# Kernel optimization log

Measured on AMD Instinct MI355X. Metric: run time of the kernel, lower is better.

Reference implementation:

```python
import jax, jax.numpy as jnp
import numpy as np

NMUL = 1
NEARZERO = 1e-5
ROUTING_LEN = 15
N_DYN = 3
N_STATIC = 13  # layout includes parRT, parAC (present in STATIC_PARAM_NAMES but unused in the step)


def _descale(x, lb, ub):
    return lb + x * (ub - lb)


def setup_inputs() -> dict:
    key = jax.random.key(0)
    k1, k2, k3 = jax.random.split(key, 3)
    T, G = 365, 50000
    u = jax.random.uniform(k1, (T, G, 3), dtype=jnp.float32)
    prcp = u[..., 0] * 10.0                 # mm/day
    tmean = (u[..., 1] - 0.3) * 20.0        # degC, roughly [-6, 14] so snow branch is exercised
    pet = u[..., 2] * 5.0                   # mm/day
    forcing = jnp.stack([prcp, tmean, pet], axis=-1)
    dyn_raw = jax.random.uniform(k2, (T, G, N_DYN * NMUL), dtype=jnp.float32)
    static_raw = jax.random.uniform(k3, (G, N_STATIC * NMUL + 2), dtype=jnp.float32)
    return {"forcing": forcing, "dyn_raw": dyn_raw, "static_raw": static_raw}


def _hbv_forward(forcing, dyn_raw, static_raw):
    T, G, _ = forcing.shape
    dt = forcing.dtype
    # --- descale dynamic params (per-timestep): parBETA, parK0, parBETAET ---
    dyn = dyn_raw.reshape(T, G, N_DYN, NMUL)
    parBETA = _descale(dyn[:, :, 0], 1.0, 6.0)
    parK0 = _descale(dyn[:, :, 1], 0.05, 0.9)
    parBETAET = _descale(dyn[:, :, 2], 0.3, 5.0)
    # --- descale static params ---
    st = static_raw[:, :N_STATIC * NMUL].reshape(G, N_STATIC, NMUL)
    parFC = _descale(st[:, 0], 50.0, 1000.0)
    parK1 = _descale(st[:, 1], 0.01, 0.5)
    parK2 = _descale(st[:, 2], 0.001, 0.2)
    parLP = _descale(st[:, 3], 0.2, 1.0)
    parPERC = _descale(st[:, 4], 0.0, 10.0)
    parUZL = _descale(st[:, 5], 0.0, 100.0)
    parTT = _descale(st[:, 6], -2.5, 2.5)
    parCFMAX = _descale(st[:, 7], 0.5, 10.0)
    parCFR = _descale(st[:, 8], 0.0, 0.1)
    parCWH = _descale(st[:, 9], 0.0, 0.2)
    parC = _descale(st[:, 10], 0.0, 1.0)
    rout = static_raw[:, N_STATIC * NMUL:]
    rout_a = _descale(rout[:, 0], 0.0, 2.9)
    rout_b = _descale(rout[:, 1], 0.0, 6.5)

    Pm = jnp.broadcast_to(forcing[..., 0:1], (T, G, NMUL))
    Tm = jnp.broadcast_to(forcing[..., 1:2], (T, G, NMUL))
    PETm = jnp.broadcast_to(forcing[..., 2:3], (T, G, NMUL))

    def step(carry, xs):
        SNOWPACK, MELTWATER, SM, SUZ, SLZ = carry
        PRECIP, TEMP, PET, pBETA, pK0, pBETAET = xs
        is_rain = (TEMP >= parTT).astype(dt)
        RAIN = PRECIP * is_rain
        SNOW = PRECIP * (1.0 - is_rain)
        SNOWPACK = SNOWPACK + SNOW
        melt = jnp.minimum(jnp.maximum(parCFMAX * (TEMP - parTT), 0.0), SNOWPACK)
        MELTWATER = MELTWATER + melt
        SNOWPACK = SNOWPACK - melt
        refreezing = jnp.minimum(jnp.maximum(parCFR * parCFMAX * (parTT - TEMP), 0.0), MELTWATER)
        SNOWPACK = SNOWPACK + refreezing
        MELTWATER = MELTWATER - refreezing
        tosoil = jnp.maximum(MELTWATER - parCWH * SNOWPACK, 0.0)
        MELTWATER = MELTWATER - tosoil
        soil_wetness = jnp.clip((SM / parFC) ** pBETA, 0.0, 1.0)
        recharge = (RAIN + tosoil) * soil_wetness
        SM = SM + RAIN + tosoil - recharge
        excess = jnp.maximum(SM - parFC, 0.0)
        SM = SM - excess
        evapfactor = jnp.clip((SM / (parLP * parFC)) ** pBETAET, 0.0, 1.0)
        ETact = jnp.minimum(SM, PET * evapfactor)
        SM = jnp.maximum(SM - ETact, NEARZERO)
        capillary = jnp.minimum(SLZ, parC * SLZ * (1.0 - jnp.minimum(SM / parFC, 1.0)))
        SM = jnp.maximum(SM + capillary, NEARZERO)
        SLZ = jnp.maximum(SLZ - capillary, NEARZERO)
        SUZ = SUZ + recharge + excess
        PERC = jnp.minimum(SUZ, parPERC)
        SUZ = SUZ - PERC
        Q0 = pK0 * jnp.maximum(SUZ - parUZL, 0.0)
        SUZ = SUZ - Q0
        Q1 = parK1 * SUZ
        SUZ = SUZ - Q1
        SLZ = jnp.maximum(SLZ + PERC, 0.0)
        Q2 = parK2 * SLZ
        SLZ = SLZ - Q2
        return (SNOWPACK, MELTWATER, SM, SUZ, SLZ), Q0 + Q1 + Q2

    init = tuple(jnp.full((G, NMUL), 0.001, dtype=dt) for _ in range(5))
    _, Qall = jax.lax.scan(step, init, (Pm, Tm, PETm, parBETA, parK0, parBETAET))
    Qsim = Qall.mean(axis=-1)  # [T, G]: average over nmul components

    # --- gamma unit-hydrograph routing (hydroDL UH_gamma + causal conv, lenF = 15) ---
    aa = jax.nn.relu(rout_a) + 0.1      # shape param, [G]
    theta = jax.nn.relu(rout_b) + 0.5   # scale param, [G]
    t = jnp.arange(0.5, ROUTING_LEN, dtype=dt)[:, None]  # [15, 1] midpoints
    w = (t ** (aa - 1.0)) * jnp.exp(-t / theta) / (jnp.exp(jax.lax.lgamma(aa)) * theta ** aa)
    w = w / w.sum(axis=0)  # [15, G], normalized UH weights
    Qpad = jnp.pad(Qsim, ((ROUTING_LEN - 1, 0), (0, 0)))
    # causal conv: Qrout[t] = sum_k w[k] * Qsim[t-k]; fixed 15-tap loop
    Qrout = sum(w[k] * jax.lax.dynamic_slice_in_dim(Qpad, ROUTING_LEN - 1 - k, T, axis=0)
                for k in range(ROUTING_LEN))
    return Qrout  # streamflow [T, G]


def reference(forcing, dyn_raw, static_raw):
    return _hbv_forward(forcing, dyn_raw, static_raw)
```

## Files before the change

### kernel.cpp

```cpp
#include <hip/hip_runtime.h>

#define NEARZERO 1e-5f
#define RLEN 15
#define LOG2E 1.4426950408889634f

struct __attribute__((packed, aligned(4))) F3 { float x, y, z; };

static __device__ __forceinline__ F3 ld3f(const float* p) {
    return *reinterpret_cast<const F3*>(p);
}

struct Par { float FC, invFC, invLPFC, K1, K2, PERC, UZL, TT, CFMAX, CFRC, CWH, C; };

template<int PH>
__device__ __forceinline__ float one_step(
    float P, float TEMP, float PET, float dx, float dy, float dz,
    const Par& pr,
    float& SNOWPACK, float& MELTWATER, float& SM, float& SUZ, float& SLZ,
    float (&acc)[RLEN], const float (&w)[RLEN])
{
    const float pBETA   = fmaf(dx, 5.0f, 1.0f);
    const float pK0     = fmaf(dy, 0.85f, 0.05f);
    const float pBETAET = fmaf(dz, 4.7f, 0.3f);

    const float d    = TEMP - pr.TT;
    const float RAIN = (d >= 0.0f) ? P : 0.0f;
    const float SNOW = P - RAIN;
    SNOWPACK += SNOW;
    const float melt = __builtin_amdgcn_fmed3f(pr.CFMAX * d, 0.0f, SNOWPACK);
    MELTWATER += melt;
    SNOWPACK  -= melt;
    const float refr = __builtin_amdgcn_fmed3f(pr.CFRC * (0.0f - d), 0.0f, MELTWATER);
    SNOWPACK  += refr;
    MELTWATER -= refr;
    const float tosoil = fmaxf(fmaf(-pr.CWH, SNOWPACK, MELTWATER), 0.0f);
    MELTWATER -= tosoil;

    const float sw = fminf(exp2f(pBETA * __log2f(SM * pr.invFC)), 1.0f);
    const float rt = RAIN + tosoil;
    const float recharge = rt * sw;
    SM = SM + rt - recharge;
    const float excess = fmaxf(SM - pr.FC, 0.0f);
    SM -= excess;
    const float ef = fminf(exp2f(pBETAET * __log2f(SM * pr.invLPFC)), 1.0f);
    const float ETact = fminf(SM, PET * ef);
    SM = fmaxf(SM - ETact, NEARZERO);
    const float capillary = pr.C * SLZ * (1.0f - fminf(SM * pr.invFC, 1.0f));
    SM  = fmaxf(SM + capillary, NEARZERO);
    SLZ = fmaxf(SLZ - capillary, NEARZERO);

    SUZ += recharge + excess;
    const float PERC = fminf(SUZ, pr.PERC);
    SUZ -= PERC;
    const float Q0 = pK0 * fmaxf(SUZ - pr.UZL, 0.0f);
    SUZ -= Q0;
    const float Q1 = pr.K1 * SUZ;
    SUZ -= Q1;
    SLZ += PERC;
    const float Q2 = pr.K2 * SLZ;
    SLZ -= Q2;
    const float Qsim = Q0 + Q1 + Q2;

    const float qr = fmaf(w[0], Qsim, acc[PH]);
    acc[PH] = 0.0f;
#pragma unroll
    for (int k = 1; k < RLEN; ++k) {
        const int j = (PH + k) % RLEN;
        acc[j] = fmaf(w[k], Qsim, acc[j]);
    }
    return qr;
}

__global__ __launch_bounds__(64, 1) void hbv_kernel(
    const float* __restrict__ forcing,
    const float* __restrict__ dynr,
    const float* __restrict__ statr,
    float* __restrict__ out,
    int G)
{
    const int lane = threadIdx.x;
    const int g  = blockIdx.x * 64 + lane;
    const int gc = (g < G) ? g : (G - 1);
    const bool guard = (g < G);

    __shared__ float ring[RLEN][64][6];

    const float* sp = statr + (size_t)gc * 15;
    Par pr;
    pr.FC    = fmaf(sp[0], 950.0f, 50.0f);
    pr.K1    = fmaf(sp[1], 0.49f, 0.01f);
    pr.K2    = fmaf(sp[2], 0.199f, 0.001f);
    const float parLP = fmaf(sp[3], 0.8f, 0.2f);
    pr.PERC  = sp[4] * 10.0f;
    pr.UZL   = sp[5] * 100.0f;
    pr.TT    = fmaf(sp[6], 5.0f, -2.5f);
    pr.CFMAX = fmaf(sp[7], 9.5f, 0.5f);
    pr.CFRC  = (sp[8] * 0.1f) * pr.CFMAX;
    pr.CWH   = sp[9] * 0.2f;
    pr.C     = sp[10];
    const float rout_a = sp[13] * 2.9f;
    const float rout_b = sp[14] * 6.5f;
    pr.invFC   = 1.0f / pr.FC;
    pr.invLPFC = 1.0f / (parLP * pr.FC);

    const float aa    = fmaxf(rout_a, 0.0f) + 0.1f;
    const float theta = fmaxf(rout_b, 0.0f) + 0.5f;
    const float am1   = aa - 1.0f;
    const float nitl2 = -LOG2E / theta;
    float w[RLEN];
    float wsum = 0.0f;
#pragma unroll
    for (int k = 0; k < RLEN; ++k) {
        const float tk = (float)k + 0.5f;
        w[k] = exp2f(am1 * __log2f(tk) + tk * nitl2);
        wsum += w[k];
    }
    const float winv = 1.0f / wsum;
#pragma unroll
    for (int k = 0; k < RLEN; ++k) w[k] *= winv;

    float SP_ = 0.001f, MW = 0.001f, SM = 0.001f, SUZ = 0.001f, SLZ = 0.001f;
    float acc[RLEN];
#pragma unroll
    for (int k = 0; k < RLEN; ++k) acc[k] = 0.0f;

    const size_t sT = (size_t)G * 3;
    const float* pF = forcing + (size_t)gc * 3;
    const float* pD = dynr    + (size_t)gc * 3;
    float* outp = out + g;

    F3 setF[5], setD[5];

    setF[1] = ld3f(pF + 4 * sT); setD[1] = ld3f(pD + 4 * sT);
    setF[2] = ld3f(pF + 5 * sT); setD[2] = ld3f(pD + 5 * sT);
    setF[3] = ld3f(pF + 6 * sT); setD[3] = ld3f(pD + 6 * sT);
    setF[4] = ld3f(pF + 7 * sT); setD[4] = ld3f(pD + 7 * sT);
#pragma unroll
    for (int r = 0; r < 4; ++r) {
        const F3 f = ld3f(pF + (size_t)r * sT);
        const F3 d = ld3f(pD + (size_t)r * sT);
        ring[r][lane][0] = f.x; ring[r][lane][1] = f.y; ring[r][lane][2] = f.z;
        ring[r][lane][3] = d.x; ring[r][lane][4] = d.y; ring[r][lane][5] = d.z;
    }

#define STEP(PH, FP, DP) do { \
    constexpr int P_  = (PH) % RLEN; \
    constexpr int S_  = P_ % 5; \
    constexpr int Sw_ = (P_ + 1) % 5; \
    constexpr int W_  = (P_ + 4) % RLEN; \
    setF[S_] = ld3f(FP); setD[S_] = ld3f(DP); \
    __builtin_amdgcn_sched_barrier(0); \
    const float P2_ = ring[P_][lane][0], T2_ = ring[P_][lane][1], E2_ = ring[P_][lane][2]; \
    const float x2_ = ring[P_][lane][3], y2_ = ring[P_][lane][4], z2_ = ring[P_][lane][5]; \
    const float qr_ = one_step<P_>(P2_, T2_, E2_, x2_, y2_, z2_, pr, \
                                   SP_, MW, SM, SUZ, SLZ, acc, w); \
    if (guard) __builtin_nontemporal_store(qr_, outp); \
    outp += G; \
    ring[W_][lane][0] = setF[Sw_].x; ring[W_][lane][1] = setF[Sw_].y; ring[W_][lane][2] = setF[Sw_].z; \
    ring[W_][lane][3] = setD[Sw_].x; ring[W_][lane][4] = setD[Sw_].y; ring[W_][lane][5] = setD[Sw_].z; \
} while (0)

    const float* pFl = pF + 8 * sT;
    const float* pDl = pD + 8 * sT;
    for (int i = 0; i < 23; ++i) {
        STEP(0,  pFl, pDl); pFl += sT; pDl += sT;
        STEP(1,  pFl, pDl); pFl += sT; pDl += sT;
        STEP(2,  pFl, pDl); pFl += sT; pDl += sT;
        STEP(3,  pFl, pDl); pFl += sT; pDl += sT;
        STEP(4,  pFl, pDl); pFl += sT; pDl += sT;
        STEP(5,  pFl, pDl); pFl += sT; pDl += sT;
        STEP(6,  pFl, pDl); pFl += sT; pDl += sT;
        STEP(7,  pFl, pDl); pFl += sT; pDl += sT;
        STEP(8,  pFl, pDl); pFl += sT; pDl += sT;
        STEP(9,  pFl, pDl); pFl += sT; pDl += sT;
        STEP(10, pFl, pDl); pFl += sT; pDl += sT;
        STEP(11, pFl, pDl); pFl += sT; pDl += sT;
        STEP(12, pFl, pDl); pFl += sT; pDl += sT;
        STEP(13, pFl, pDl); pFl += sT; pDl += sT;
        STEP(14, pFl, pDl); pFl += sT; pDl += sT;
    }
#define TROW(T) (((T) + 8 <= 364) ? ((T) + 8) : 364)
    STEP(0,  pF + (size_t)TROW(345) * sT, pD + (size_t)TROW(345) * sT);
    STEP(1,  pF + (size_t)TROW(346) * sT, pD + (size_t)TROW(346) * sT);
    STEP(2,  pF + (size_t)TROW(347) * sT, pD + (size_t)TROW(347) * sT);
    STEP(3,  pF + (size_t)TROW(348) * sT, pD + (size_t)TROW(348) * sT);
    STEP(4,  pF + (size_t)TROW(349) * sT, pD + (size_t)TROW(349) * sT);
    STEP(5,  pF + (size_t)TROW(350) * sT, pD + (size_t)TROW(350) * sT);
    STEP(6,  pF + (size_t)TROW(351) * sT, pD + (size_t)TROW(351) * sT);
    STEP(7,  pF + (size_t)TROW(352) * sT, pD + (size_t)TROW(352) * sT);
    STEP(8,  pF + (size_t)TROW(353) * sT, pD + (size_t)TROW(353) * sT);
    STEP(9,  pF + (size_t)TROW(354) * sT, pD + (size_t)TROW(354) * sT);
    STEP(10, pF + (size_t)TROW(355) * sT, pD + (size_t)TROW(355) * sT);
    STEP(11, pF + (size_t)TROW(356) * sT, pD + (size_t)TROW(356) * sT);
    STEP(12, pF + (size_t)TROW(357) * sT, pD + (size_t)TROW(357) * sT);
    STEP(13, pF + (size_t)TROW(358) * sT, pD + (size_t)TROW(358) * sT);
    STEP(14, pF + (size_t)TROW(359) * sT, pD + (size_t)TROW(359) * sT);
    STEP(0,  pF + (size_t)TROW(360) * sT, pD + (size_t)TROW(360) * sT);
    STEP(1,  pF + (size_t)TROW(361) * sT, pD + (size_t)TROW(361) * sT);
    STEP(2,  pF + (size_t)TROW(362) * sT, pD + (size_t)TROW(362) * sT);
    STEP(3,  pF + (size_t)TROW(363) * sT, pD + (size_t)TROW(363) * sT);
    STEP(4,  pF + (size_t)TROW(364) * sT, pD + (size_t)TROW(364) * sT);
#undef TROW
#undef STEP
}

extern "C" void kernel_launch(void* const* d_in, const int* in_sizes, int n_in,
                              void* d_out, int out_size, void* d_ws, size_t ws_size,
                              hipStream_t stream) {
    const float* forcing = (const float*)d_in[0];
    const float* dynr    = (const float*)d_in[1];
    const float* statr   = (const float*)d_in[2];
    float* out = (float*)d_out;

    const int G = in_sizes[2] / 15;
    const int block = 64;
    const int grid  = (G + block - 1) / block;
    hbv_kernel<<<grid, block, 0, stream>>>(forcing, dynr, statr, out, G);
}
```

Before: 111.2 us.

## Replace LDS ring prefetch with 3-deep register prefetch of forcing inputs

Removes the shared-memory ring buffer that staged forcing and dynamic parameters eight steps ahead. Inputs now go through a three-slot register buffer that is reloaded right after each step consumes it, so prefetch distance drops from eight steps to three. This cuts LDS traffic and the per-step write/read round trip, and the sched_barrier mask is relaxed so the compiler has more scheduling freedom. The cost is less latency hiding for global loads, which could expose memory latency given only one wave per block.

```diff
diff --git a/kernel.cpp b/kernel.cpp
--- a/kernel.cpp
+++ b/kernel.cpp
@@ -5,7 +5,6 @@
 #define LOG2E 1.4426950408889634f
 
 struct __attribute__((packed, aligned(4))) F3 { float x, y, z; };
-
 static __device__ __forceinline__ F3 ld3f(const float* p) {
     return *reinterpret_cast<const F3*>(p);
 }
@@ -14,19 +13,17 @@
 
 template<int PH>
 __device__ __forceinline__ float one_step(
-    float P, float TEMP, float PET, float dx, float dy, float dz,
-    const Par& pr,
+    const F3& f, const F3& d3, const Par& pr,
     float& SNOWPACK, float& MELTWATER, float& SM, float& SUZ, float& SLZ,
     float (&acc)[RLEN], const float (&w)[RLEN])
 {
-    const float pBETA   = fmaf(dx, 5.0f, 1.0f);
-    const float pK0     = fmaf(dy, 0.85f, 0.05f);
-    const float pBETAET = fmaf(dz, 4.7f, 0.3f);
+    const float pBETA   = fmaf(d3.x, 5.0f, 1.0f);
+    const float pK0     = fmaf(d3.y, 0.85f, 0.05f);
+    const float pBETAET = fmaf(d3.z, 4.7f, 0.3f);
 
-    const float d    = TEMP - pr.TT;
-    const float RAIN = (d >= 0.0f) ? P : 0.0f;
-    const float SNOW = P - RAIN;
-    SNOWPACK += SNOW;
+    const float d    = f.y - pr.TT;
+    const float RAIN = (d >= 0.0f) ? f.x : 0.0f;
+    SNOWPACK += f.x - RAIN;
     const float melt = __builtin_amdgcn_fmed3f(pr.CFMAX * d, 0.0f, SNOWPACK);
     MELTWATER += melt;
     SNOWPACK  -= melt;
@@ -43,7 +40,7 @@
     const float excess = fmaxf(SM - pr.FC, 0.0f);
     SM -= excess;
     const float ef = fminf(exp2f(pBETAET * __log2f(SM * pr.invLPFC)), 1.0f);
-    const float ETact = fminf(SM, PET * ef);
+    const float ETact = fminf(SM, f.z * ef);
     SM = fmaxf(SM - ETact, NEARZERO);
     const float capillary = pr.C * SLZ * (1.0f - fminf(SM * pr.invFC, 1.0f));
     SM  = fmaxf(SM + capillary, NEARZERO);
@@ -71,19 +68,17 @@
     return qr;
 }
 
-__global__ __launch_bounds__(64, 1) void hbv_kernel(
-    const float* __restrict__ forcing,
-    const float* __restrict__ dynr,
-    const float* __restrict__ statr,
-    float* __restrict__ out,
-    int G)
+__global__ __launch_bounds__(64, 1)
+void hbv_kernel(const float* __restrict__ forcing,
+                const float* __restrict__ dynr,
+                const float* __restrict__ statr,
+                float* __restrict__ out,
+                int G)
 {
     const int lane = threadIdx.x;
     const int g  = blockIdx.x * 64 + lane;
     const int gc = (g < G) ? g : (G - 1);
     const bool guard = (g < G);
-
-    __shared__ float ring[RLEN][64][6];
 
     const float* sp = statr + (size_t)gc * 15;
     Par pr;
@@ -127,80 +122,45 @@
     const size_t sT = (size_t)G * 3;
     const float* pF = forcing + (size_t)gc * 3;
     const float* pD = dynr    + (size_t)gc * 3;
+
+    F3 bF[3], bD[3];
+    bF[0] = ld3f(pF);          bD[0] = ld3f(pD);
+    bF[1] = ld3f(pF + sT);     bD[1] = ld3f(pD + sT);
+    bF[2] = ld3f(pF + 2 * sT); bD[2] = ld3f(pD + 2 * sT);
+
+    const float* rF = pF + 3 * sT;
+    const float* rD = pD + 3 * sT;
     float* outp = out + g;
 
-    F3 setF[5], setD[5];
-
-    setF[1] = ld3f(pF + 4 * sT); setD[1] = ld3f(pD + 4 * sT);
-    setF[2] = ld3f(pF + 5 * sT); setD[2] = ld3f(pD + 5 * sT);
-    setF[3] = ld3f(pF + 6 * sT); setD[3] = ld3f(pD + 6 * sT);
-    setF[4] = ld3f(pF + 7 * sT); setD[4] = ld3f(pD + 7 * sT);
-#pragma unroll
-    for (int r = 0; r < 4; ++r) {
-        const F3 f = ld3f(pF + (size_t)r * sT);
-        const F3 d = ld3f(pD + (size_t)r * sT);
-        ring[r][lane][0] = f.x; ring[r][lane][1] = f.y; ring[r][lane][2] = f.z;
-        ring[r][lane][3] = d.x; ring[r][lane][4] = d.y; ring[r][lane][5] = d.z;
-    }
-
 #define STEP(PH, FP, DP) do { \
-    constexpr int P_  = (PH) % RLEN; \
-    constexpr int S_  = P_ % 5; \
-    constexpr int Sw_ = (P_ + 1) % 5; \
-    constexpr int W_  = (P_ + 4) % RLEN; \
-    setF[S_] = ld3f(FP); setD[S_] = ld3f(DP); \
-    __builtin_amdgcn_sched_barrier(0); \
-    const float P2_ = ring[P_][lane][0], T2_ = ring[P_][lane][1], E2_ = ring[P_][lane][2]; \
-    const float x2_ = ring[P_][lane][3], y2_ = ring[P_][lane][4], z2_ = ring[P_][lane][5]; \
-    const float qr_ = one_step<P_>(P2_, T2_, E2_, x2_, y2_, z2_, pr, \
+    constexpr int P_ = (PH) % RLEN; \
+    constexpr int S_ = P_ % 3; \
+    const float qr_ = one_step<P_>(bF[S_], bD[S_], pr, \
                                    SP_, MW, SM, SUZ, SLZ, acc, w); \
+    bF[S_] = ld3f(FP); bD[S_] = ld3f(DP); \
+    __builtin_amdgcn_sched_barrier(0x7); \
     if (guard) __builtin_nontemporal_store(qr_, outp); \
     outp += G; \
-    ring[W_][lane][0] = setF[Sw_].x; ring[W_][lane][1] = setF[Sw_].y; ring[W_][lane][2] = setF[Sw_].z; \
-    ring[W_][lane][3] = setD[Sw_].x; ring[W_][lane][4] = setD[Sw_].y; ring[W_][lane][5] = setD[Sw_].z; \
 } while (0)
 
-    const float* pFl = pF + 8 * sT;
-    const float* pDl = pD + 8 * sT;
-    for (int i = 0; i < 23; ++i) {
-        STEP(0,  pFl, pDl); pFl += sT; pDl += sT;
-        STEP(1,  pFl, pDl); pFl += sT; pDl += sT;
-        STEP(2,  pFl, pDl); pFl += sT; pDl += sT;
-        STEP(3,  pFl, pDl); pFl += sT; pDl += sT;
-        STEP(4,  pFl, pDl); pFl += sT; pDl += sT;
-        STEP(5,  pFl, pDl); pFl += sT; pDl += sT;
-        STEP(6,  pFl, pDl); pFl += sT; pDl += sT;
-        STEP(7,  pFl, pDl); pFl += sT; pDl += sT;
-        STEP(8,  pFl, pDl); pFl += sT; pDl += sT;
-        STEP(9,  pFl, pDl); pFl += sT; pDl += sT;
-        STEP(10, pFl, pDl); pFl += sT; pDl += sT;
-        STEP(11, pFl, pDl); pFl += sT; pDl += sT;
-        STEP(12, pFl, pDl); pFl += sT; pDl += sT;
-        STEP(13, pFl, pDl); pFl += sT; pDl += sT;
-        STEP(14, pFl, pDl); pFl += sT; pDl += sT;
+#define STEPADV(PH) do { \
+    STEP(PH, rF, rD); \
+    rF += sT; rD += sT; \
+} while (0)
+
+    for (int i = 0; i < 24; ++i) {
+        STEPADV(0);  STEPADV(1);  STEPADV(2);  STEPADV(3);  STEPADV(4);
+        STEPADV(5);  STEPADV(6);  STEPADV(7);  STEPADV(8);  STEPADV(9);
+        STEPADV(10); STEPADV(11); STEPADV(12); STEPADV(13); STEPADV(14);
     }
-#define TROW(T) (((T) + 8 <= 364) ? ((T) + 8) : 364)
-    STEP(0,  pF + (size_t)TROW(345) * sT, pD + (size_t)TROW(345) * sT);
-    STEP(1,  pF + (size_t)TROW(346) * sT, pD + (size_t)TROW(346) * sT);
-    STEP(2,  pF + (size_t)TROW(347) * sT, pD + (size_t)TROW(347) * sT);
-    STEP(3,  pF + (size_t)TROW(348) * sT, pD + (size_t)TROW(348) * sT);
-    STEP(4,  pF + (size_t)TROW(349) * sT, pD + (size_t)TROW(349) * sT);
-    STEP(5,  pF + (size_t)TROW(350) * sT, pD + (size_t)TROW(350) * sT);
-    STEP(6,  pF + (size_t)TROW(351) * sT, pD + (size_t)TROW(351) * sT);
-    STEP(7,  pF + (size_t)TROW(352) * sT, pD + (size_t)TROW(352) * sT);
-    STEP(8,  pF + (size_t)TROW(353) * sT, pD + (size_t)TROW(353) * sT);
-    STEP(9,  pF + (size_t)TROW(354) * sT, pD + (size_t)TROW(354) * sT);
-    STEP(10, pF + (size_t)TROW(355) * sT, pD + (size_t)TROW(355) * sT);
-    STEP(11, pF + (size_t)TROW(356) * sT, pD + (size_t)TROW(356) * sT);
-    STEP(12, pF + (size_t)TROW(357) * sT, pD + (size_t)TROW(357) * sT);
-    STEP(13, pF + (size_t)TROW(358) * sT, pD + (size_t)TROW(358) * sT);
-    STEP(14, pF + (size_t)TROW(359) * sT, pD + (size_t)TROW(359) * sT);
-    STEP(0,  pF + (size_t)TROW(360) * sT, pD + (size_t)TROW(360) * sT);
-    STEP(1,  pF + (size_t)TROW(361) * sT, pD + (size_t)TROW(361) * sT);
-    STEP(2,  pF + (size_t)TROW(362) * sT, pD + (size_t)TROW(362) * sT);
-    STEP(3,  pF + (size_t)TROW(363) * sT, pD + (size_t)TROW(363) * sT);
-    STEP(4,  pF + (size_t)TROW(364) * sT, pD + (size_t)TROW(364) * sT);
-#undef TROW
+#define TR(T) ((((T) + 3) <= 364) ? ((T) + 3) : 364)
+    STEP(0, pF + (size_t)TR(360) * sT, pD + (size_t)TR(360) * sT);
+    STEP(1, pF + (size_t)TR(361) * sT, pD + (size_t)TR(361) * sT);
+    STEP(2, pF + (size_t)TR(362) * sT, pD + (size_t)TR(362) * sT);
+    STEP(3, pF + (size_t)TR(363) * sT, pD + (size_t)TR(363) * sT);
+    STEP(4, pF + (size_t)TR(364) * sT, pD + (size_t)TR(364) * sT);
+#undef TR
+#undef STEPADV
 #undef STEP
 }
 
```

Result: slower. 114.1 us (+2.6%).
